# Optimization experiments

Hardware: AMD Instinct MI355X
Metric: run time of the kernel (lower is better)

The kernel has to match this reference:

```python
import jax, jax.numpy as jnp
import numpy as np
from jax import lax

B, M, N = 4096, 306, 984
LAMBDA = 0.1
MAX_ITER = 50


def setup_inputs() -> dict:
    key = jax.random.key(0)
    k1, k2, k3, k4 = jax.random.split(key, 4)
    return {
        "r_real": jax.random.normal(k1, (B, M), dtype=jnp.float32),
        "r_imag": jax.random.normal(k2, (B, M), dtype=jnp.float32),
        # phi buffer: torch.randn(M, N, dtype=complex64) -> real/imag each ~N(0, 1/2)?
        # torch.randn(complex64) draws real & imag each from N(0, 1/sqrt(2)^2)=N(0,0.5).
        "phi_real": jax.random.normal(k3, (M, N), dtype=jnp.float32) * np.float32(1.0 / np.sqrt(2.0)),
        "phi_imag": jax.random.normal(k4, (M, N), dtype=jnp.float32) * np.float32(1.0 / np.sqrt(2.0)),
    }


def reference(r_real, r_imag, phi_real, phi_imag):
    phi = (phi_real + 1j * phi_imag).astype(jnp.complex64)          # [M, N]
    r = (r_real + 1j * r_imag).astype(jnp.complex64)                # [B, M]
    # step_size = 1 / ||phi||_2^2  (spectral norm squared)
    step = (1.0 / jnp.linalg.norm(phi, ord=2) ** 2).real.astype(jnp.float32)
    thresh = (LAMBDA * step).astype(jnp.float32)
    phi_c = jnp.conj(phi)

    def body(w, _):
        # error = w @ phi.T - r : [B, M]
        error = jnp.einsum("bn,mn->bm", w, phi) - r
        # gradient = error @ conj(phi) : [B, N]
        grad = jnp.einsum("bm,mn->bn", error, phi_c)
        w_next = w - step * grad
        w_mag = jnp.abs(w_next)
        new_mag = jax.nn.relu(w_mag - thresh)
        # polar(new_mag, angle(w_next))
        w_new = (new_mag * jnp.exp(1j * jnp.angle(w_next))).astype(jnp.complex64)
        return w_new, None

    w0 = jnp.zeros((r.shape[0], N), dtype=jnp.complex64)
    w, _ = lax.scan(body, w0, None, length=MAX_ITER)
    return jnp.abs(w).astype(jnp.float32)
```

## Files before the change

kernel.cpp:

```cpp
#include <hip/hip_runtime.h>
#include <math.h>

#define Bb 4096
#define Mm 306
#define Nn 984
#define NCP 1024
#define KA 2048
#define ITERS 50
#define KSQ 9

typedef _Float16 f16x8 __attribute__((ext_vector_type(8)));
typedef float f32x16 __attribute__((ext_vector_type(16)));

__device__ __forceinline__ void cmac(float2& c, const float2 a, const float2 b) {
    c.x = fmaf(a.x, b.x, c.x);
    c.x = fmaf(-a.y, b.y, c.x);
    c.y = fmaf(a.x, b.y, c.y);
    c.y = fmaf(a.y, b.x, c.y);
}

__device__ __forceinline__ unsigned short f16bits(float v) {
    union { _Float16 h; unsigned short u; } cv;
    cv.h = (_Float16)v;
    return cv.u;
}
__device__ __forceinline__ float f16lo(unsigned int u) {
    union { unsigned short s; _Float16 h; } cv; cv.s = (unsigned short)(u & 0xffffu);
    return (float)cv.h;
}
__device__ __forceinline__ float f16hi(unsigned int u) {
    union { unsigned short s; _Float16 h; } cv; cv.s = (unsigned short)(u >> 16);
    return (float)cv.h;
}

__device__ __forceinline__ void load_lds16(const void* g, void* l) {
    __builtin_amdgcn_global_load_lds((const __attribute__((address_space(1))) void*)g,
                                     (__attribute__((address_space(3))) void*)l, 16, 0, 0);
}

__device__ __forceinline__ size_t swzA(int b, int c) {
    return ((size_t)(((b >> 7) * 32 + (c >> 5)) * 1024 + ((c >> 2) & 7) * 128 + (b & 127))) * 4 + (c & 3);
}
__device__ __forceinline__ size_t swzB(int jr, int q) {
    return ((size_t)(((jr >> 7) * 32 + (q >> 5)) * 1024 + ((q >> 2) & 7) * 128 + (jr & 127))) * 4 + (q & 3);
}
__device__ __forceinline__ size_t swzA2(int b, int c) {
    return ((size_t)(((b >> 7) * 10 + (c >> 5)) * 1024 + ((c >> 2) & 7) * 128 + (b & 127))) * 4 + (c & 3);
}
__device__ __forceinline__ size_t swzB2(int jr, int q) {
    return ((size_t)(((jr >> 7) * 10 + (q >> 5)) * 1024 + ((q >> 2) & 7) * 128 + (jr & 127))) * 4 + (q & 3);
}

__global__ void gram_kernel(const float* __restrict__ pr, const float* __restrict__ pi,
                            float2* __restrict__ G) {
    int j = blockIdx.x * 16 + threadIdx.x;
    int i = blockIdx.y * 16 + threadIdx.y;
    if (i >= Mm || j >= Mm) return;
    const float* pri = pr + (size_t)i * Nn;
    const float* pii = pi + (size_t)i * Nn;
    const float* prj = pr + (size_t)j * Nn;
    const float* pij = pi + (size_t)j * Nn;
    float ar = 0.f, ai = 0.f;
    for (int n = 0; n < Nn; ++n) {
        float xr = pri[n], xi = pii[n], yr = prj[n], yi = pij[n];
        ar = fmaf(xr, yr, ar); ar = fmaf(xi, yi, ar);
        ai = fmaf(xi, yr, ai); ai = fmaf(-xr, yi, ai);
    }
    G[i * Mm + j] = make_float2(ar, ai);
}

__global__ void frob_kernel(const float2* __restrict__ H, float* __restrict__ slot, int n) {
    int idx = blockIdx.x * blockDim.x + threadIdx.x;
    int stride = gridDim.x * blockDim.x;
    float s = 0.f;
    for (int i = idx; i < n; i += stride) {
        float2 v = H[i];
        s = fmaf(v.x, v.x, s);
        s = fmaf(v.y, v.y, s);
    }
    #pragma unroll
    for (int o = 32; o > 0; o >>= 1) s += __shfl_down(s, o, 64);
    __shared__ float wsum[4];
    int lane = threadIdx.x & 63, wv = threadIdx.x >> 6;
    if (lane == 0) wsum[wv] = s;
    __syncthreads();
    if (threadIdx.x == 0) atomicAdd(slot, wsum[0] + wsum[1] + wsum[2] + wsum[3]);
}

__global__ void sqmm_kernel(const float2* __restrict__ A, float2* __restrict__ C,
                            const float* __restrict__ fslot) {
    __shared__ float2 As[32][33];
    __shared__ float2 Bs[32][33];
    float inv = 1.0f / fslot[0];
    int tx = threadIdx.x, ty = threadIdx.y;
    int t = ty * 16 + tx;
    int r0 = blockIdx.y * 32, c0 = blockIdx.x * 32;
    int zs = blockIdx.z * 80;
    int ze = zs + 80 < Mm ? zs + 80 : Mm;
    float2 acc[2][2] = {};
    for (int k0 = zs; k0 < ze; k0 += 32) {
        #pragma unroll
        for (int i = 0; i < 4; ++i) {
            int idx = t + i * 256;
            int rr = idx >> 5, cc = idx & 31;
            int gr = r0 + rr, gk = k0 + cc;
            As[rr][cc] = (gr < Mm && gk < ze) ? A[gr * Mm + gk] : make_float2(0.f, 0.f);
            int gk2 = k0 + rr, gc = c0 + cc;
            Bs[rr][cc] = (gk2 < ze && gc < Mm) ? A[gk2 * Mm + gc] : make_float2(0.f, 0.f);
        }
        __syncthreads();
        #pragma unroll 8
        for (int kk = 0; kk < 32; ++kk) {
            float2 a0 = As[ty * 2][kk], a1 = As[ty * 2 + 1][kk];
            float2 b0 = Bs[kk][tx * 2], b1 = Bs[kk][tx * 2 + 1];
            cmac(acc[0][0], a0, b0); cmac(acc[0][1], a0, b1);
            cmac(acc[1][0], a1, b0); cmac(acc[1][1], a1, b1);
        }
        __syncthreads();
    }
    #pragma unroll
    for (int i = 0; i < 2; ++i) {
        int gr = r0 + ty * 2 + i;
        #pragma unroll
        for (int j = 0; j < 2; ++j) {
            int gc = c0 + tx * 2 + j;
            if (gr < Mm && gc < Mm) {
                atomicAdd(&C[gr * Mm + gc].x, acc[i][j].x * inv);
                atomicAdd(&C[gr * Mm + gc].y, acc[i][j].y * inv);
            }
        }
    }
}

__global__ void rayleigh_kernel(const float2* __restrict__ H, const float2* __restrict__ G,
                                float* __restrict__ sc) {
    __shared__ float2 v[Mm];
    __shared__ float rn[320], rd[320];
    int t = threadIdx.x;
    if (t < Mm) {
        float2 s = make_float2(0.f, 0.f);
        for (int j = 0; j < Mm; ++j) { float2 h = H[t * Mm + j]; s.x += h.x; s.y += h.y; }
        v[t] = s;
    }
    __syncthreads();
    float num = 0.f, den = 0.f;
    if (t < Mm) {
        float2 u = make_float2(0.f, 0.f);
        for (int k = 0; k < Mm; ++k) {
            float2 g = G[k * Mm + t];
            float2 vk = v[k];
            u.x = fmaf(g.x, vk.x, u.x); u.x = fmaf(g.y, vk.y, u.x);
            u.y = fmaf(g.x, vk.y, u.y); u.y = fmaf(-g.y, vk.x, u.y);
        }
        float2 vt = v[t];
        num = vt.x * u.x + vt.y * u.y;
        den = vt.x * vt.x + vt.y * vt.y;
    }
    rn[t] = num; rd[t] = den;
    __syncthreads();
    if (t == 0) {
        float sn = 0.f, sd = 0.f;
        for (int i = 0; i < 320; ++i) { sn += rn[i]; sd += rd[i]; }
        float lam = sn / sd;
        float step = 1.0f / lam;
        sc[0] = step;
        sc[1] = 0.1f * step;
    }
}

__global__ void qpack_kernel(const float* __restrict__ pr, const float* __restrict__ pi,
                             unsigned int* __restrict__ Bu, const float* __restrict__ sc) {
    __shared__ float2 Pn[16][33];
    __shared__ float2 Pc[16][33];
    float nstep = -sc[0];
    int t = threadIdx.x;
    int tx = t & 15, ty = t >> 4;
    int n0 = blockIdx.x * 32, c0 = blockIdx.y * 32;
    float2 q[2][2] = {};
    for (int m0 = 0; m0 < Mm; m0 += 16) {
        #pragma unroll
        for (int rep = 0; rep < 2; ++rep) {
            int idx = t + rep * 256;
            int mm = idx >> 5, col = idx & 31;
            int gm = m0 + mm;
            float2 a = make_float2(0.f, 0.f), b = make_float2(0.f, 0.f);
            if (gm < Mm) {
                if (n0 + col < Nn) a = make_float2(pr[(size_t)gm * Nn + n0 + col], pi[(size_t)gm * Nn + n0 + col]);
                if (c0 + col < Nn) b = make_float2(pr[(size_t)gm * Nn + c0 + col], pi[(size_t)gm * Nn + c0 + col]);
            }
            Pn[mm][col] = a; Pc[mm][col] = b;
        }
        __syncthreads();
        #pragma unroll
        for (int mm = 0; mm < 16; ++mm) {
            float2 a0 = Pn[mm][ty * 2], a1 = Pn[mm][ty * 2 + 1];
            float2 b0 = Pc[mm][tx * 2], b1 = Pc[mm][tx * 2 + 1];
            #define QMAC(qq, aa, bb) \
                qq.x = fmaf(aa.x, bb.x, qq.x); qq.x = fmaf(aa.y, bb.y, qq.x); \
                qq.y = fmaf(aa.y, bb.x, qq.y); qq.y = fmaf(-aa.x, bb.y, qq.y);
            QMAC(q[0][0], a0, b0) QMAC(q[0][1], a0, b1)
            QMAC(q[1][0], a1, b0) QMAC(q[1][1], a1, b1)
            #undef QMAC
        }
        __syncthreads();
    }
    #pragma unroll
    for (int i = 0; i < 2; ++i) {
        int n = n0 + ty * 2 + i;
        #pragma unroll
        for (int j = 0; j < 2; ++j) {
            int c = c0 + tx * 2 + j;
            if (n < Nn && c < Nn) {
                float MR = nstep * q[i][j].x, MI = nstep * q[i][j].y;
                unsigned short hR = f16bits(MR);
                unsigned short hI = f16bits(MI);
                unsigned short nhI = hI ^ 0x8000u;
                int jr = ((c >> 5) * 64) + (c & 31);
                Bu[swzB(jr, n)]      = (unsigned)hR | ((unsigned)nhI << 16);
                Bu[swzB(jr + 32, n)] = (unsigned)hI | ((unsigned)hR << 16);
            }
        }
    }
}

__global__ void rpack_kernel(const float* __restrict__ rr, const float* __restrict__ ri,
                             unsigned int* __restrict__ rp16) {
    int b = blockIdx.x * 256 + threadIdx.x;
    int m = blockIdx.y;
    rp16[swzA2(b, m)] = (unsigned)f16bits(rr[(size_t)b * Mm + m]) |
                        ((unsigned)f16bits(ri[(size_t)b * Mm + m]) << 16);
}

__global__ void ppack2_kernel(const float* __restrict__ pr, const float* __restrict__ pi,
                              unsigned int* __restrict__ B2u, const float* __restrict__ sc) {
    int n = blockIdx.x * 256 + threadIdx.x;
    int m = blockIdx.y;
    if (n >= Nn) return;
    float s = sc[0];
    float xr = pr[(size_t)m * Nn + n], xi = pi[(size_t)m * Nn + n];
    unsigned short x = f16bits(-s * xr), y = f16bits(-s * xi);
    int jr2 = ((n >> 5) * 64) + (n & 31);
    B2u[swzB2(jr2, m)]      = (unsigned)x | ((unsigned)y << 16);
    B2u[swzB2(jr2 + 32, m)] = (unsigned)(y ^ 0x8000u) | ((unsigned)x << 16);
}

__global__ __launch_bounds__(256, 2) void rphi_mfma_kernel(
    const _Float16* __restrict__ rp16, const _Float16* __restrict__ B2,
    unsigned int* __restrict__ rph16) {
    __shared__ _Float16 As[8192];
    __shared__ _Float16 Bs[8192];
    int tid = threadIdx.x;
    int lane = tid & 63, wv = tid >> 6;
    int wm = wv & 1, wn = wv >> 1;
    int bblk = blockIdx.x, nblk = blockIdx.y;
    int l31 = lane & 31, lh = lane >> 5;

    f32x16 acc[2][2] = {};

    for (int kt = 0; kt < 10; ++kt) {
        #pragma unroll
        for (int c = 0; c < 4; ++c) {
            int u = c * 256 + tid;
            const char* ga = (const char*)rp16 + (((size_t)(bblk * 10 + kt)) * 1024 + u) * 16;
            load_lds16(ga, &As[(size_t)(c * 256 + wv * 64) * 8]);
            const char* gb = (const char*)B2 + (((size_t)(nblk * 10 + kt)) * 1024 + u) * 16;
            load_lds16(gb, &Bs[(size_t)(c * 256 + wv * 64) * 8]);
        }
        __syncthreads();
        #pragma unroll
        for (int s = 0; s < 4; ++s) {
            int kq = s * 2 + lh;
            f16x8 af[2], bfr[2];
            #pragma unroll
            for (int mt = 0; mt < 2; ++mt)
                af[mt] = *reinterpret_cast<const f16x8*>(
                    &As[(size_t)(kq * 128 + wm * 64 + mt * 32 + l31) * 8]);
            #pragma unroll
            for (int nt = 0; nt < 2; ++nt)
                bfr[nt] = *reinterpret_cast<const f16x8*>(
                    &Bs[(size_t)(kq * 128 + wn * 64 + nt * 32 + l31) * 8]);
            #pragma unroll
            for (int mt = 0; mt < 2; ++mt)
                #pragma unroll
                for (int nt = 0; nt < 2; ++nt)
                    acc[mt][nt] = __builtin_amdgcn_mfma_f32_32x32x16_f16(af[mt], bfr[nt], acc[mt][nt], 0, 0, 0);
        }
        __syncthreads();
    }

    int b0 = bblk * 128;
    int c = nblk * 64 + wn * 32 + l31;
    #pragma unroll
    for (int mt = 0; mt < 2; ++mt) {
        #pragma unroll
        for (int reg = 0; reg < 16; ++reg) {
            int row = b0 + wm * 64 + mt * 32 + ((reg & 3) + 8 * (reg >> 2) + 4 * lh);
            rph16[(size_t)row * NCP + c] =
                (unsigned)f16bits(-acc[mt][0][reg]) | ((unsigned)f16bits(-acc[mt][1][reg]) << 16);
        }
    }
}

__global__ __launch_bounds__(256, 2) void ista7_kernel(
    const _Float16* __restrict__ wfi, const _Float16* __restrict__ Bq,
    unsigned int* __restrict__ wfo,
    const unsigned int* __restrict__ rph16,
    const float* __restrict__ sc, float* __restrict__ out, int last) {
    __shared__ _Float16 As[8192];
    __shared__ _Float16 Bs[8192];
    int tid = threadIdx.x;
    int lane = tid & 63, wv = tid >> 6;
    int wm = wv & 1, wn = wv >> 1;
    int id = blockIdx.x;
    int bblk = id >> 4;
    int nblk = id & 15;
    int l31 = lane & 31, lh = lane >> 5;

    f32x16 acc[2][2] = {};

    for (int kt = 0; kt < 32; ++kt) {
        #pragma unroll
        for (int c = 0; c < 4; ++c) {
            int u = c * 256 + tid;
            const char* ga = (const char*)wfi + (((size_t)(bblk * 32 + kt)) * 1024 + u) * 16;
            load_lds16(ga, &As[(size_t)(c * 256 + wv * 64) * 8]);
            const char* gb = (const char*)Bq + (((size_t)(nblk * 32 + kt)) * 1024 + u) * 16;
            load_lds16(gb, &Bs[(size_t)(c * 256 + wv * 64) * 8]);
        }
        __syncthreads();
        #pragma unroll
        for (int s = 0; s < 4; ++s) {
            int kq = s * 2 + lh;
            f16x8 af[2], bfr[2];
            #pragma unroll
            for (int mt = 0; mt < 2; ++mt)
                af[mt] = *reinterpret_cast<const f16x8*>(
                    &As[(size_t)(kq * 128 + wm * 64 + mt * 32 + l31) * 8]);
            #pragma unroll
            for (int nt = 0; nt < 2; ++nt)
                bfr[nt] = *reinterpret_cast<const f16x8*>(
                    &Bs[(size_t)(kq * 128 + wn * 64 + nt * 32 + l31) * 8]);
            #pragma unroll
            for (int mt = 0; mt < 2; ++mt)
                #pragma unroll
                for (int nt = 0; nt < 2; ++nt)
                    acc[mt][nt] = __builtin_amdgcn_mfma_f32_32x32x16_f16(af[mt], bfr[nt], acc[mt][nt], 0, 0, 0);
        }
        __syncthreads();
    }

    float thr = sc[1];
    int b0 = bblk * 128;
    int c = nblk * 64 + wn * 32 + l31;
    const unsigned int* wfin = (const unsigned int*)wfi;
    #pragma unroll
    for (int mt = 0; mt < 2; ++mt) {
        #pragma unroll
        for (int reg = 0; reg < 16; ++reg) {
            int row = b0 + wm * 64 + mt * 32 + ((reg & 3) + 8 * (reg >> 2) + 4 * lh);
            unsigned int wu = wfin[swzA(row, c)];
            unsigned int ru = rph16[(size_t)row * NCP + c];
            float zr = f16lo(wu) + acc[mt][0][reg] + f16lo(ru);
            float zi = f16hi(wu) + acc[mt][1][reg] + f16hi(ru);
            float mag = sqrtf(zr * zr + zi * zi);
            float nm = mag - thr;
            float f = (nm > 0.f) ? (nm / mag) : 0.f;
            wfo[swzA(row, c)] = (unsigned)f16bits(zr * f) | ((unsigned)f16bits(zi * f) << 16);
            if (last && c < Nn) out[(size_t)row * Nn + c] = fmaxf(nm, 0.f);
        }
    }
}

extern "C" void kernel_launch(void* const* d_in, const int* in_sizes, int n_in,
                              void* d_out, int out_size, void* d_ws, size_t ws_size,
                              hipStream_t stream) {
    const float* rr = (const float*)d_in[0];
    const float* ri = (const float*)d_in[1];
    const float* pr = (const float*)d_in[2];
    const float* pi = (const float*)d_in[3];
    float* out = (float*)d_out;

    char* ws = (char*)d_ws;
    size_t off = 0;
    _Float16* wf0 = (_Float16*)(ws + off); off += (size_t)Bb * KA * sizeof(_Float16);
    _Float16* wf1 = (_Float16*)(ws + off); off += (size_t)Bb * KA * sizeof(_Float16);
    _Float16* Bq  = (_Float16*)(ws + off); off += (size_t)2048 * 2048 * sizeof(_Float16);
    unsigned int* rph16 = (unsigned int*)(ws + off); off += (size_t)Bb * NCP * 4;
    _Float16* rp16 = (_Float16*)(ws + off); off += (size_t)Bb * 640 * sizeof(_Float16);
    _Float16* B2  = (_Float16*)(ws + off); off += (size_t)2048 * 640 * sizeof(_Float16);
    float2* G = (float2*)(ws + off);     off += (size_t)Mm * Mm * sizeof(float2);
    float2* H1 = (float2*)(ws + off);    off += (size_t)Mm * Mm * sizeof(float2);
    float2* H2 = (float2*)(ws + off);    off += (size_t)Mm * Mm * sizeof(float2);
    float* slots = (float*)(ws + off);   off += 64 * sizeof(float);
    float* sc = slots + 32;

    (void)hipMemsetAsync(wf0, 0, (size_t)Bb * KA * sizeof(_Float16), stream);
    (void)hipMemsetAsync(Bq, 0, (size_t)2048 * 2048 * sizeof(_Float16), stream);
    (void)hipMemsetAsync(rp16, 0, (size_t)Bb * 640 * sizeof(_Float16), stream);
    (void)hipMemsetAsync(B2, 0, (size_t)2048 * 640 * sizeof(_Float16), stream);
    (void)hipMemsetAsync(slots, 0, 64 * sizeof(float), stream);

    gram_kernel<<<dim3(20, 20), dim3(16, 16), 0, stream>>>(pr, pi, G);
    float2* bufs[2] = { H1, H2 };
    const float2* src = G;
    for (int s = 0; s < KSQ; ++s) {
        frob_kernel<<<128, 256, 0, stream>>>(src, slots + s, Mm * Mm);
        float2* dst = bufs[s & 1];
        (void)hipMemsetAsync(dst, 0, (size_t)Mm * Mm * sizeof(float2), stream);
        sqmm_kernel<<<dim3(10, 10, 4), dim3(16, 16), 0, stream>>>(src, dst, slots + s);
        src = dst;
    }
    rayleigh_kernel<<<1, 320, 0, stream>>>(src, G, sc);

    qpack_kernel<<<dim3(31, 31), 256, 0, stream>>>(pr, pi, (unsigned int*)Bq, sc);
    rpack_kernel<<<dim3(16, Mm), 256, 0, stream>>>(rr, ri, (unsigned int*)rp16);
    ppack2_kernel<<<dim3(4, Mm), 256, 0, stream>>>(pr, pi, (unsigned int*)B2, sc);
    rphi_mfma_kernel<<<dim3(32, 16), 256, 0, stream>>>(rp16, B2, rph16);

    _Float16* wbuf[2] = { wf0, wf1 };
    for (int it = 0; it < ITERS; ++it) {
        ista7_kernel<<<512, 256, 0, stream>>>(
            wbuf[it & 1], Bq, (unsigned int*)wbuf[(it + 1) & 1], rph16, sc, out,
            it == ITERS - 1 ? 1 : 0);
    }
}
```

Baseline: 3.120 ms.

## Double-buffer LDS tiles in MFMA kernels and tile the Gram kernel with split-K

The rphi and ISTA MFMA kernels now keep two LDS buffers. The next K-tile's global-to-LDS loads are issued before computing on the current tile, so load latency overlaps with MFMA work and one barrier per iteration goes away. The Gram-matrix kernel changes from a naive per-thread dot product to a 32x32 shared-memory tiled kernel with a 2x2 register block. It splits K four ways and combines partial sums with float atomics into a pre-zeroed G. The cost is double the LDS per block, which may limit occupancy, plus nondeterministic summation order in G.

```diff
diff --git a/kernel.cpp b/kernel.cpp
--- a/kernel.cpp
+++ b/kernel.cpp
@@ -53,20 +53,54 @@
 
 __global__ void gram_kernel(const float* __restrict__ pr, const float* __restrict__ pi,
                             float2* __restrict__ G) {
-    int j = blockIdx.x * 16 + threadIdx.x;
-    int i = blockIdx.y * 16 + threadIdx.y;
-    if (i >= Mm || j >= Mm) return;
-    const float* pri = pr + (size_t)i * Nn;
-    const float* pii = pi + (size_t)i * Nn;
-    const float* prj = pr + (size_t)j * Nn;
-    const float* pij = pi + (size_t)j * Nn;
-    float ar = 0.f, ai = 0.f;
-    for (int n = 0; n < Nn; ++n) {
-        float xr = pri[n], xi = pii[n], yr = prj[n], yi = pij[n];
-        ar = fmaf(xr, yr, ar); ar = fmaf(xi, yi, ar);
-        ai = fmaf(xi, yr, ai); ai = fmaf(-xr, yi, ai);
-    }
-    G[i * Mm + j] = make_float2(ar, ai);
+    __shared__ float2 As[32][33];
+    __shared__ float2 Bs[32][33];
+    int tx = threadIdx.x, ty = threadIdx.y;
+    int t = ty * 16 + tx;
+    int i0 = blockIdx.y * 32, j0 = blockIdx.x * 32;
+    int zs = blockIdx.z * 246;
+    int ze = zs + 246 < Nn ? zs + 246 : Nn;
+    float2 acc[2][2] = {};
+    for (int k0 = zs; k0 < ze; k0 += 32) {
+        #pragma unroll
+        for (int rep = 0; rep < 4; ++rep) {
+            int idx = t + rep * 256;
+            int rr = idx >> 5, cc = idx & 31;
+            int gk = k0 + cc;
+            int gi = i0 + rr, gj = j0 + rr;
+            float2 a = make_float2(0.f, 0.f), b = make_float2(0.f, 0.f);
+            if (gk < ze) {
+                if (gi < Mm) a = make_float2(pr[(size_t)gi * Nn + gk], pi[(size_t)gi * Nn + gk]);
+                if (gj < Mm) b = make_float2(pr[(size_t)gj * Nn + gk], pi[(size_t)gj * Nn + gk]);
+            }
+            As[rr][cc] = a; Bs[rr][cc] = b;
+        }
+        __syncthreads();
+        #pragma unroll 8
+        for (int kk = 0; kk < 32; ++kk) {
+            float2 a0 = As[ty * 2][kk], a1 = As[ty * 2 + 1][kk];
+            float2 b0 = Bs[tx * 2][kk], b1 = Bs[tx * 2 + 1][kk];
+            #define GMAC(qq, aa, bb) \
+                qq.x = fmaf(aa.x, bb.x, qq.x); qq.x = fmaf(aa.y, bb.y, qq.x); \
+                qq.y = fmaf(aa.y, bb.x, qq.y); qq.y = fmaf(-aa.x, bb.y, qq.y);
+            GMAC(acc[0][0], a0, b0) GMAC(acc[0][1], a0, b1)
+            GMAC(acc[1][0], a1, b0) GMAC(acc[1][1], a1, b1)
+            #undef GMAC
+        }
+        __syncthreads();
+    }
+    #pragma unroll
+    for (int i = 0; i < 2; ++i) {
+        int gi = i0 + ty * 2 + i;
+        #pragma unroll
+        for (int j = 0; j < 2; ++j) {
+            int gj = j0 + tx * 2 + j;
+            if (gi < Mm && gj < Mm) {
+                atomicAdd(&G[gi * Mm + gj].x, acc[i][j].x);
+                atomicAdd(&G[gi * Mm + gj].y, acc[i][j].y);
+            }
+        }
+    }
 }
 
 __global__ void frob_kernel(const float2* __restrict__ H, float* __restrict__ slot, int n) {
@@ -247,8 +281,8 @@
 __global__ __launch_bounds__(256, 2) void rphi_mfma_kernel(
     const _Float16* __restrict__ rp16, const _Float16* __restrict__ B2,
     unsigned int* __restrict__ rph16) {
-    __shared__ _Float16 As[8192];
-    __shared__ _Float16 Bs[8192];
+    __shared__ _Float16 As[2][8192];
+    __shared__ _Float16 Bs[2][8192];
     int tid = threadIdx.x;
     int lane = tid & 63, wv = tid >> 6;
     int wm = wv & 1, wn = wv >> 1;
@@ -257,16 +291,29 @@
 
     f32x16 acc[2][2] = {};
 
+    const char* gabase = (const char*)rp16 + ((size_t)bblk * 10 * 1024) * 16;
+    const char* gbbase = (const char*)B2 + ((size_t)nblk * 10 * 1024) * 16;
+
+    #pragma unroll
+    for (int c = 0; c < 4; ++c) {
+        int u = c * 256 + tid;
+        load_lds16(gabase + (size_t)u * 16, &As[0][(size_t)(c * 256 + wv * 64) * 8]);
+        load_lds16(gbbase + (size_t)u * 16, &Bs[0][(size_t)(c * 256 + wv * 64) * 8]);
+    }
+    __syncthreads();
+
     for (int kt = 0; kt < 10; ++kt) {
-        #pragma unroll
-        for (int c = 0; c < 4; ++c) {
-            int u = c * 256 + tid;
-            const char* ga = (const char*)rp16 + (((size_t)(bblk * 10 + kt)) * 1024 + u) * 16;
-            load_lds16(ga, &As[(size_t)(c * 256 + wv * 64) * 8]);
-            const char* gb = (const char*)B2 + (((size_t)(nblk * 10 + kt)) * 1024 + u) * 16;
-            load_lds16(gb, &Bs[(size_t)(c * 256 + wv * 64) * 8]);
-        }
-        __syncthreads();
+        int cur = kt & 1;
+        if (kt + 1 < 10) {
+            #pragma unroll
+            for (int c = 0; c < 4; ++c) {
+                int u = c * 256 + tid;
+                load_lds16(gabase + ((size_t)(kt + 1) * 1024 + u) * 16,
+                           &As[cur ^ 1][(size_t)(c * 256 + wv * 64) * 8]);
+                load_lds16(gbbase + ((size_t)(kt + 1) * 1024 + u) * 16,
+                           &Bs[cur ^ 1][(size_t)(c * 256 + wv * 64) * 8]);
+            }
+        }
         #pragma unroll
         for (int s = 0; s < 4; ++s) {
             int kq = s * 2 + lh;
@@ -274,11 +321,11 @@
             #pragma unroll
             for (int mt = 0; mt < 2; ++mt)
                 af[mt] = *reinterpret_cast<const f16x8*>(
-                    &As[(size_t)(kq * 128 + wm * 64 + mt * 32 + l31) * 8]);
+                    &As[cur][(size_t)(kq * 128 + wm * 64 + mt * 32 + l31) * 8]);
             #pragma unroll
             for (int nt = 0; nt < 2; ++nt)
                 bfr[nt] = *reinterpret_cast<const f16x8*>(
-                    &Bs[(size_t)(kq * 128 + wn * 64 + nt * 32 + l31) * 8]);
+                    &Bs[cur][(size_t)(kq * 128 + wn * 64 + nt * 32 + l31) * 8]);
             #pragma unroll
             for (int mt = 0; mt < 2; ++mt)
                 #pragma unroll
@@ -306,8 +353,8 @@
     unsigned int* __restrict__ wfo,
     const unsigned int* __restrict__ rph16,
     const float* __restrict__ sc, float* __restrict__ out, int last) {
-    __shared__ _Float16 As[8192];
-    __shared__ _Float16 Bs[8192];
+    __shared__ _Float16 As[2][8192];
+    __shared__ _Float16 Bs[2][8192];
     int tid = threadIdx.x;
     int lane = tid & 63, wv = tid >> 6;
     int wm = wv & 1, wn = wv >> 1;
@@ -318,16 +365,29 @@
 
     f32x16 acc[2][2] = {};
 
+    const char* gabase = (const char*)wfi + ((size_t)bblk * 32 * 1024) * 16;
+    const char* gbbase = (const char*)Bq + ((size_t)nblk * 32 * 1024) * 16;
+
+    #pragma unroll
+    for (int c = 0; c < 4; ++c) {
+        int u = c * 256 + tid;
+        load_lds16(gabase + (size_t)u * 16, &As[0][(size_t)(c * 256 + wv * 64) * 8]);
+        load_lds16(gbbase + (size_t)u * 16, &Bs[0][(size_t)(c * 256 + wv * 64) * 8]);
+    }
+    __syncthreads();
+
     for (int kt = 0; kt < 32; ++kt) {
-        #pragma unroll
-        for (int c = 0; c < 4; ++c) {
-            int u = c * 256 + tid;
-            const char* ga = (const char*)wfi + (((size_t)(bblk * 32 + kt)) * 1024 + u) * 16;
-            load_lds16(ga, &As[(size_t)(c * 256 + wv * 64) * 8]);
-            const char* gb = (const char*)Bq + (((size_t)(nblk * 32 + kt)) * 1024 + u) * 16;
-            load_lds16(gb, &Bs[(size_t)(c * 256 + wv * 64) * 8]);
-        }
-        __syncthreads();
+        int cur = kt & 1;
+        if (kt + 1 < 32) {
+            #pragma unroll
+            for (int c = 0; c < 4; ++c) {
+                int u = c * 256 + tid;
+                load_lds16(gabase + ((size_t)(kt + 1) * 1024 + u) * 16,
+                           &As[cur ^ 1][(size_t)(c * 256 + wv * 64) * 8]);
+                load_lds16(gbbase + ((size_t)(kt + 1) * 1024 + u) * 16,
+                           &Bs[cur ^ 1][(size_t)(c * 256 + wv * 64) * 8]);
+            }
+        }
         #pragma unroll
         for (int s = 0; s < 4; ++s) {
             int kq = s * 2 + lh;
@@ -335,11 +395,11 @@
             #pragma unroll
             for (int mt = 0; mt < 2; ++mt)
                 af[mt] = *reinterpret_cast<const f16x8*>(
-                    &As[(size_t)(kq * 128 + wm * 64 + mt * 32 + l31) * 8]);
+                    &As[cur][(size_t)(kq * 128 + wm * 64 + mt * 32 + l31) * 8]);
             #pragma unroll
             for (int nt = 0; nt < 2; ++nt)
                 bfr[nt] = *reinterpret_cast<const f16x8*>(
-                    &Bs[(size_t)(kq * 128 + wn * 64 + nt * 32 + l31) * 8]);
+                    &Bs[cur][(size_t)(kq * 128 + wn * 64 + nt * 32 + l31) * 8]);
             #pragma unroll
             for (int mt = 0; mt < 2; ++mt)
                 #pragma unroll
@@ -399,8 +459,9 @@
     (void)hipMemsetAsync(rp16, 0, (size_t)Bb * 640 * sizeof(_Float16), stream);
     (void)hipMemsetAsync(B2, 0, (size_t)2048 * 640 * sizeof(_Float16), stream);
     (void)hipMemsetAsync(slots, 0, 64 * sizeof(float), stream);
-
-    gram_kernel<<<dim3(20, 20), dim3(16, 16), 0, stream>>>(pr, pi, G);
+    (void)hipMemsetAsync(G, 0, (size_t)Mm * Mm * sizeof(float2), stream);
+
+    gram_kernel<<<dim3(10, 10, 4), dim3(16, 16), 0, stream>>>(pr, pi, G);
     float2* bufs[2] = { H1, H2 };
     const float2* src = G;
     for (int s = 0; s < KSQ; ++s) {
```

New measurement: 3.183 ms. 2.0% more time.
